# Kernel tuning notes

Measured on AMD Instinct MI355X. Metric: run time of the kernel, lower is better.

The kernel has to match this reference:

```python
import jax, jax.numpy as jnp
import numpy as np

N_NODES = 100000
N_EDGES = 1600000
IN_CH, HID_CH, OUT_CH = 128, 128, 64


def setup_inputs() -> dict:
    key = jax.random.key(0)
    k_x, k_e, k1, k2, k3 = jax.random.split(key, 5)
    x = jax.random.normal(k_x, (N_NODES, IN_CH), dtype=jnp.float32)
    edge_index = jax.random.randint(k_e, (2, N_EDGES), 0, N_NODES, dtype=jnp.int64)
    # Glorot-ish init for the three GCNConv weight matrices (no bias).
    W1 = jax.random.normal(k1, (IN_CH, HID_CH), dtype=jnp.float32) / np.sqrt(IN_CH)
    W2 = jax.random.normal(k2, (HID_CH, HID_CH), dtype=jnp.float32) / np.sqrt(HID_CH)
    W3 = jax.random.normal(k3, (HID_CH, OUT_CH), dtype=jnp.float32) / np.sqrt(HID_CH)
    return {"x": x, "edge_index": edge_index, "W1": W1, "W2": W2, "W3": W3}


def _gcn_layer(x, src, dst, W):
    # GCNConv(normalize=False, bias=False): transform then sum-aggregate over edges.
    h = x @ W                      # [N, d_out]
    msgs = h[src]                  # [E, d_out] gather from source nodes
    return jax.ops.segment_sum(msgs, dst, num_segments=N_NODES)  # scatter-add to targets


def reference(x, edge_index, W1, W2, W3):
    src, dst = edge_index[0], edge_index[1]  # PyG flow: source_to_target
    h = _gcn_layer(x, src, dst, W1)
    h = _gcn_layer(h, src, dst, W2)
    h = _gcn_layer(h, src, dst, W3)
    return h  # [N, OUT_CH]
```

## Files before the change

kernel.cpp:

```cpp
#include <hip/hip_runtime.h>

#define N_NODES 100000
#define N_EDGES 1600000
#define CAP 48
#define NBUCK 256
#define NPB 391
#define SCAP 8192
#define NREP 4
#define SCAP4 (SCAP / NREP)
#define EPB 4096
#define NBIN ((N_EDGES + EPB - 1) / EPB)

typedef unsigned int uint;
typedef unsigned short ushort;

__device__ __forceinline__ void fma4(float4& c, float s, const float4& w) {
    c.x += s * w.x; c.y += s * w.y; c.z += s * w.z; c.w += s * w.w;
}

__device__ __forceinline__ ushort bf16r(float f) {
    union { float f; uint u; } v; v.f = f;
    return (ushort)((v.u + 0x7fffu + ((v.u >> 16) & 1u)) >> 16);
}

struct alignas(16) GemmSmem {
    float Xs[128][36];
    float Ws[32][64];
};

template <typename OutT>
__device__ __forceinline__ void gemm64_block(GemmSmem& sm, int bid,
                                             const float* __restrict__ X,
                                             const float* __restrict__ W,
                                             OutT* __restrict__ H, int n) {
    const int tid  = threadIdx.x;
    const int row0 = bid * 128;
    const int rg   = tid >> 4;
    const int cg   = tid & 15;

    float4 acc0[8];
#pragma unroll
    for (int r = 0; r < 8; r++) acc0[r] = make_float4(0.f, 0.f, 0.f, 0.f);

    const int lr = tid >> 1;
    const int lh = tid & 1;
    int grow = row0 + lr; if (grow > n - 1) grow = n - 1;
    const float* gx_base = X + (size_t)grow * 128 + lh * 16;

    for (int k0 = 0; k0 < 128; k0 += 32) {
        const float* gx = gx_base + k0;
#pragma unroll
        for (int i = 0; i < 4; i++)
            *(float4*)&sm.Xs[lr][lh * 16 + 4 * i] = *(const float4*)(gx + 4 * i);
        const float4* gw = (const float4*)(W + (size_t)k0 * 64);
        float4* sw = (float4*)&sm.Ws[0][0];
#pragma unroll
        for (int i = 0; i < 2; i++) sw[tid + 256 * i] = gw[tid + 256 * i];
        __syncthreads();

#pragma unroll
        for (int kk = 0; kk < 32; kk += 4) {
            float4 w00 = *(const float4*)&sm.Ws[kk + 0][cg * 4];
            float4 w01 = *(const float4*)&sm.Ws[kk + 1][cg * 4];
            float4 w02 = *(const float4*)&sm.Ws[kk + 2][cg * 4];
            float4 w03 = *(const float4*)&sm.Ws[kk + 3][cg * 4];
#pragma unroll
            for (int r = 0; r < 8; r++) {
                float4 a = *(const float4*)&sm.Xs[rg + 16 * r][kk];
                fma4(acc0[r], a.x, w00);
                fma4(acc0[r], a.y, w01);
                fma4(acc0[r], a.z, w02);
                fma4(acc0[r], a.w, w03);
            }
        }
        __syncthreads();
    }

#pragma unroll
    for (int r = 0; r < 8; r++) {
        int row = row0 + rg + 16 * r;
        if (row < n) {
            if constexpr (sizeof(OutT) == 2) {
                ushort4 o0 = make_ushort4(bf16r(acc0[r].x), bf16r(acc0[r].y),
                                          bf16r(acc0[r].z), bf16r(acc0[r].w));
                *(ushort4*)&H[(size_t)row * 64 + cg * 4] = o0;
            } else {
                *(float4*)&H[(size_t)row * 64 + cg * 4] = *(float4*)&acc0[r];
            }
        }
    }
}

union BinWcSmem {
    struct {
        int ecnt[NBUCK];
        int base[NBUCK];
        int lofs[NBUCK];
        uint2 estage[EPB];
    } b;
    GemmSmem g;
};

__global__ void __launch_bounds__(256) bin_wc(const int* __restrict__ src,
                                              const int* __restrict__ dst,
                                              int* __restrict__ gcur,
                                              uint2* __restrict__ seg, int E,
                                              const float* __restrict__ W1,
                                              const float* __restrict__ W2,
                                              const float* __restrict__ W3,
                                              float* __restrict__ W23,
                                              float* __restrict__ Wc) {
    __shared__ BinWcSmem sh;
    if (blockIdx.x == gridDim.x - 1) {
        gemm64_block<float>(sh.g, 0, W2, W3, W23, 128);
        __syncthreads();
        gemm64_block<float>(sh.g, 0, W1, W23, Wc, 128);
        return;
    }
    const int t = threadIdx.x;
    sh.b.ecnt[t] = 0;
    __syncthreads();
    const int e0 = blockIdx.x * EPB;
    const int rep = blockIdx.x & (NREP - 1);
    uint sreg[EPB / 256];
    int  dreg[EPB / 256];
    int  slreg[EPB / 256];
#pragma unroll
    for (int k = 0; k < EPB / 256; k++) {
        int i = e0 + k * 256 + t;
        if (i < E) {
            int d = dst[i];
            sreg[k] = (uint)src[i];
            dreg[k] = d;
            slreg[k] = atomicAdd(&sh.b.ecnt[d / NPB], 1);
        }
    }
    __syncthreads();
    const int c = sh.b.ecnt[t];
    sh.b.base[t] = (c > 0) ? atomicAdd(&gcur[rep * NBUCK + t], c) : 0;
    sh.b.lofs[t] = c;
    __syncthreads();
#pragma unroll
    for (int off = 1; off < NBUCK; off <<= 1) {
        int u = (t >= off) ? sh.b.lofs[t - off] : 0;
        __syncthreads();
        sh.b.lofs[t] += u;
        __syncthreads();
    }
    const int excl = sh.b.lofs[t] - c;
    __syncthreads();
    sh.b.lofs[t] = excl;
    __syncthreads();
#pragma unroll
    for (int k = 0; k < EPB / 256; k++) {
        int i = e0 + k * 256 + t;
        if (i < E) {
            int b = dreg[k] / NPB;
            sh.b.estage[sh.b.lofs[b] + slreg[k]] =
                make_uint2(sreg[k], (uint)dreg[k]);
        }
    }
    __syncthreads();
    const int total = min(E - e0, EPB);
    for (int i = t; i < total; i += 256) {
        uint2 e = sh.b.estage[i];
        int b = (int)e.y / NPB;
        int s = sh.b.base[b] + (i - sh.b.lofs[b]);
        if (s < SCAP4)
            seg[(size_t)b * SCAP + rep * SCAP4 + s] = e;
    }
}

union CsrGemmSmem {
    int lc[NPB];
    GemmSmem g;
};

__global__ void __launch_bounds__(256, 3) csr_gemm(const int* __restrict__ gcur,
                                                   const uint2* __restrict__ seg,
                                                   int* __restrict__ col,
                                                   int* __restrict__ cnt,
                                                   const float* __restrict__ X,
                                                   const float* __restrict__ Wc,
                                                   ushort* __restrict__ Y, int n) {
    __shared__ CsrGemmSmem sh;
    if (blockIdx.x < NBUCK) {
        const int b = blockIdx.x;
        const int t = threadIdx.x;
        for (int i = t; i < NPB; i += 256) sh.lc[i] = 0;
        __syncthreads();
        const int node0 = b * NPB;
#pragma unroll
        for (int q = 0; q < NREP; q++) {
            int m = gcur[q * NBUCK + b]; if (m > SCAP4) m = SCAP4;
            const uint2* sg = seg + (size_t)b * SCAP + q * SCAP4;
            for (int i = t; i < m; i += 256) {
                uint2 e = sg[i];
                int d = (int)e.y;
                int slot = atomicAdd(&sh.lc[d - node0], 1);
                if (slot < CAP) col[(size_t)d * CAP + slot] = (int)e.x;
            }
        }
        __syncthreads();
        for (int i = t; i < NPB; i += 256) {
            int node = node0 + i;
            if (node < n) cnt[node] = (sh.lc[i] > CAP) ? CAP : sh.lc[i];
        }
    } else {
        gemm64_block<ushort>(sh.g, blockIdx.x - NBUCK, X, Wc, Y, n);
    }
}

__device__ __forceinline__ float2 bf2f(uint u) {
    union { uint u; float f; } a, b;
    a.u = u << 16; b.u = u & 0xffff0000u;
    return make_float2(a.f, b.f);
}

template <bool FINAL>
__global__ void __launch_bounds__(256) agg64(const uint4* __restrict__ T_in,
                                             const int* __restrict__ cnt,
                                             const int* __restrict__ col,
                                             void* __restrict__ T_out, int n) {
    int gid  = blockIdx.x * blockDim.x + threadIdx.x;
    int node = gid >> 3;
    int lane = gid & 7;
    if (node >= n) return;
    int m = cnt[node]; if (m > CAP) m = CAP;
    const int* cb = col + (size_t)node * CAP;
    const uint4* tb = T_in + lane;
    float4 accA = make_float4(0.f, 0.f, 0.f, 0.f);
    float4 accB = make_float4(0.f, 0.f, 0.f, 0.f);
    int j = 0;
    for (; j + 8 <= m; j += 8) {
        int4 c0 = *(const int4*)&cb[j];
        int4 c1 = *(const int4*)&cb[j + 4];
        uint4 u0 = tb[(size_t)c0.x * 8];
        uint4 u1 = tb[(size_t)c0.y * 8];
        uint4 u2 = tb[(size_t)c0.z * 8];
        uint4 u3 = tb[(size_t)c0.w * 8];
        uint4 u4 = tb[(size_t)c1.x * 8];
        uint4 u5 = tb[(size_t)c1.y * 8];
        uint4 u6 = tb[(size_t)c1.z * 8];
        uint4 u7 = tb[(size_t)c1.w * 8];
        float2 p0 = bf2f(u0.x), p1 = bf2f(u1.x), p2 = bf2f(u2.x), p3 = bf2f(u3.x);
        float2 p4 = bf2f(u4.x), p5 = bf2f(u5.x), p6 = bf2f(u6.x), p7 = bf2f(u7.x);
        accA.x += ((p0.x + p1.x) + (p2.x + p3.x)) + ((p4.x + p5.x) + (p6.x + p7.x));
        accA.y += ((p0.y + p1.y) + (p2.y + p3.y)) + ((p4.y + p5.y) + (p6.y + p7.y));
        float2 q0 = bf2f(u0.y), q1 = bf2f(u1.y), q2 = bf2f(u2.y), q3 = bf2f(u3.y);
        float2 q4 = bf2f(u4.y), q5 = bf2f(u5.y), q6 = bf2f(u6.y), q7 = bf2f(u7.y);
        accA.z += ((q0.x + q1.x) + (q2.x + q3.x)) + ((q4.x + q5.x) + (q6.x + q7.x));
        accA.w += ((q0.y + q1.y) + (q2.y + q3.y)) + ((q4.y + q5.y) + (q6.y + q7.y));
        float2 r0 = bf2f(u0.z), r1 = bf2f(u1.z), r2 = bf2f(u2.z), r3 = bf2f(u3.z);
        float2 r4 = bf2f(u4.z), r5 = bf2f(u5.z), r6 = bf2f(u6.z), r7 = bf2f(u7.z);
        accB.x += ((r0.x + r1.x) + (r2.x + r3.x)) + ((r4.x + r5.x) + (r6.x + r7.x));
        accB.y += ((r0.y + r1.y) + (r2.y + r3.y)) + ((r4.y + r5.y) + (r6.y + r7.y));
        float2 s0 = bf2f(u0.w), s1 = bf2f(u1.w), s2 = bf2f(u2.w), s3 = bf2f(u3.w);
        float2 s4 = bf2f(u4.w), s5 = bf2f(u5.w), s6 = bf2f(u6.w), s7 = bf2f(u7.w);
        accB.z += ((s0.x + s1.x) + (s2.x + s3.x)) + ((s4.x + s5.x) + (s6.x + s7.x));
        accB.w += ((s0.y + s1.y) + (s2.y + s3.y)) + ((s4.y + s5.y) + (s6.y + s7.y));
    }
    for (; j + 4 <= m; j += 4) {
        int4 c0 = *(const int4*)&cb[j];
        uint4 u0 = tb[(size_t)c0.x * 8];
        uint4 u1 = tb[(size_t)c0.y * 8];
        uint4 u2 = tb[(size_t)c0.z * 8];
        uint4 u3 = tb[(size_t)c0.w * 8];
        float2 p0 = bf2f(u0.x), p1 = bf2f(u1.x), p2 = bf2f(u2.x), p3 = bf2f(u3.x);
        accA.x += (p0.x + p1.x) + (p2.x + p3.x);
        accA.y += (p0.y + p1.y) + (p2.y + p3.y);
        float2 q0 = bf2f(u0.y), q1 = bf2f(u1.y), q2 = bf2f(u2.y), q3 = bf2f(u3.y);
        accA.z += (q0.x + q1.x) + (q2.x + q3.x);
        accA.w += (q0.y + q1.y) + (q2.y + q3.y);
        float2 r0 = bf2f(u0.z), r1 = bf2f(u1.z), r2 = bf2f(u2.z), r3 = bf2f(u3.z);
        accB.x += (r0.x + r1.x) + (r2.x + r3.x);
        accB.y += (r0.y + r1.y) + (r2.y + r3.y);
        float2 s0 = bf2f(u0.w), s1 = bf2f(u1.w), s2 = bf2f(u2.w), s3 = bf2f(u3.w);
        accB.z += (s0.x + s1.x) + (s2.x + s3.x);
        accB.w += (s0.y + s1.y) + (s2.y + s3.y);
    }
    for (; j < m; j++) {
        uint4 u = tb[(size_t)cb[j] * 8];
        float2 p = bf2f(u.x), q = bf2f(u.y), r = bf2f(u.z), s = bf2f(u.w);
        accA.x += p.x; accA.y += p.y; accA.z += q.x; accA.w += q.y;
        accB.x += r.x; accB.y += r.y; accB.z += s.x; accB.w += s.y;
    }
    if (FINAL) {
        ((float4*)T_out)[(size_t)node * 16 + lane * 2]     = accA;
        ((float4*)T_out)[(size_t)node * 16 + lane * 2 + 1] = accB;
    } else {
        uint4 o;
        o.x = (uint)bf16r(accA.x) | ((uint)bf16r(accA.y) << 16);
        o.y = (uint)bf16r(accA.z) | ((uint)bf16r(accA.w) << 16);
        o.z = (uint)bf16r(accB.x) | ((uint)bf16r(accB.y) << 16);
        o.w = (uint)bf16r(accB.z) | ((uint)bf16r(accB.w) << 16);
        ((uint4*)T_out)[(size_t)node * 8 + lane] = o;
    }
}


static inline size_t align_up(size_t x, size_t a) { return (x + a - 1) & ~(a - 1); }

extern "C" void kernel_launch(void* const* d_in, const int* in_sizes, int n_in,
                              void* d_out, int out_size, void* d_ws, size_t ws_size,
                              hipStream_t stream) {
    const float* x  = (const float*)d_in[0];
    const int*   ei = (const int*)d_in[1];
    const float* W1 = (const float*)d_in[2];
    const float* W2 = (const float*)d_in[3];
    const float* W3 = (const float*)d_in[4];
    float* out = (float*)d_out;

    const int N = N_NODES;
    const int E = N_EDGES;
    const int* src = ei;
    const int* dst = ei + E;

    char* p = (char*)d_ws;
    int*    gcur = (int*)p;   p += align_up((size_t)NREP * NBUCK * 4, 256);
    int*    cnt  = (int*)p;   p += align_up((size_t)N * 4, 256);
    uint2*  seg  = (uint2*)p; p += align_up((size_t)NBUCK * SCAP * 8, 256);
    int*    col  = (int*)p;   p += align_up((size_t)N * CAP * 4, 256);
    float*  W23  = (float*)p; p += align_up((size_t)128 * 64 * 4, 256);
    float*  Wc   = (float*)p; p += align_up((size_t)128 * 64 * 4, 256);
    ushort* Y    = (ushort*)p; p += align_up((size_t)N * 64 * 2, 256);
    ushort* Za   = (ushort*)p; p += align_up((size_t)N * 64 * 2, 256);

    hipMemsetAsync(gcur, 0, (size_t)NREP * NBUCK * 4, stream);

    bin_wc<<<NBIN + 1, 256, 0, stream>>>(src, dst, gcur, seg, E,
                                         W1, W2, W3, W23, Wc);

    const int gemm_blocks = (N + 127) / 128;
    csr_gemm<<<NBUCK + gemm_blocks, 256, 0, stream>>>(gcur, seg, col, cnt,
                                                      x, Wc, Y, N);

    const int agg_blocks = (N * 8 + 255) / 256;
    agg64<false><<<agg_blocks, 256, 0, stream>>>((const uint4*)Y,  cnt, col, Za, N);
    agg64<false><<<agg_blocks, 256, 0, stream>>>((const uint4*)Za, cnt, col, Y,  N);
    agg64<true ><<<agg_blocks, 256, 0, stream>>>((const uint4*)Y,  cnt, col, out, N);
}
```

Measured before the change: 251.1 us.

## Replace padded ELL neighbor lists with compact per-bucket CSR rowptr layout

The CSR build now counts in-degrees per bucket first, runs a shared-memory prefix scan (each degree rounded up to a multiple of 4 for int4 loads), and writes neighbor indices compactly into a per-bucket region with a rowptr array, instead of fixed 48-slot padded rows per node. The aggregation kernels read neighbor lists through rowptr. This shrinks the col array and improves cache and DRAM locality of the index reads in the three aggregation passes. In exchange the build does a second pass over the binned edges, an extra scan with several barriers, and one more indirection load per node.

```diff
diff --git a/kernel.cpp b/kernel.cpp
--- a/kernel.cpp
+++ b/kernel.cpp
@@ -172,7 +172,11 @@
 }
 
 union CsrGemmSmem {
-    int lc[NPB];
+    struct {
+        int lc[NPB];
+        int lrp[NPB];
+        int sc[2][512];
+    } c;
     GemmSmem g;
 };
 
@@ -180,6 +184,7 @@
                                                    const uint2* __restrict__ seg,
                                                    int* __restrict__ col,
                                                    int* __restrict__ cnt,
+                                                   int* __restrict__ rowptr,
                                                    const float* __restrict__ X,
                                                    const float* __restrict__ Wc,
                                                    ushort* __restrict__ Y, int n) {
@@ -187,24 +192,59 @@
     if (blockIdx.x < NBUCK) {
         const int b = blockIdx.x;
         const int t = threadIdx.x;
-        for (int i = t; i < NPB; i += 256) sh.lc[i] = 0;
-        __syncthreads();
         const int node0 = b * NPB;
+        for (int i = t; i < NPB; i += 256) sh.c.lc[i] = 0;
+        __syncthreads();
+#pragma unroll
+        for (int q = 0; q < NREP; q++) {
+            int m = gcur[q * NBUCK + b]; if (m > SCAP4) m = SCAP4;
+            const uint2* sg = seg + (size_t)b * SCAP + q * SCAP4;
+            for (int i = t; i < m; i += 256)
+                atomicAdd(&sh.c.lc[(int)sg[i].y - node0], 1);
+        }
+        __syncthreads();
+        sh.c.sc[0][t]       = (t < NPB) ? ((sh.c.lc[t] + 3) & ~3) : 0;
+        sh.c.sc[0][t + 256] = (t + 256 < NPB) ? ((sh.c.lc[t + 256] + 3) & ~3) : 0;
+        __syncthreads();
+        int pb = 0;
+#pragma unroll
+        for (int off = 1; off < 512; off <<= 1) {
+            int a0 = sh.c.sc[pb][t];
+            int a1 = sh.c.sc[pb][t + 256];
+            int b0 = (t >= off) ? sh.c.sc[pb][t - off] : 0;
+            int b1 = (t + 256 >= off) ? sh.c.sc[pb][t + 256 - off] : 0;
+            sh.c.sc[pb ^ 1][t]       = a0 + b0;
+            sh.c.sc[pb ^ 1][t + 256] = a1 + b1;
+            __syncthreads();
+            pb ^= 1;
+        }
+        if (t < NPB)
+            sh.c.lrp[t] = sh.c.sc[pb][t] - ((sh.c.lc[t] + 3) & ~3);
+        if (t + 256 < NPB)
+            sh.c.lrp[t + 256] = sh.c.sc[pb][t + 256] - ((sh.c.lc[t + 256] + 3) & ~3);
+        __syncthreads();
+        for (int i = t; i < NPB; i += 256) sh.c.lc[i] = 0;
+        __syncthreads();
 #pragma unroll
         for (int q = 0; q < NREP; q++) {
             int m = gcur[q * NBUCK + b]; if (m > SCAP4) m = SCAP4;
             const uint2* sg = seg + (size_t)b * SCAP + q * SCAP4;
             for (int i = t; i < m; i += 256) {
                 uint2 e = sg[i];
-                int d = (int)e.y;
-                int slot = atomicAdd(&sh.lc[d - node0], 1);
-                if (slot < CAP) col[(size_t)d * CAP + slot] = (int)e.x;
+                int dn = (int)e.y - node0;
+                int slot = atomicAdd(&sh.c.lc[dn], 1);
+                int pos = sh.c.lrp[dn] + slot;
+                if (pos < SCAP) col[(size_t)b * SCAP + pos] = (int)e.x;
             }
         }
         __syncthreads();
         for (int i = t; i < NPB; i += 256) {
             int node = node0 + i;
-            if (node < n) cnt[node] = (sh.lc[i] > CAP) ? CAP : sh.lc[i];
+            if (node < n) {
+                int c = sh.c.lc[i];
+                cnt[node] = (c > CAP) ? CAP : c;
+                rowptr[node] = b * SCAP + sh.c.lrp[i];
+            }
         }
     } else {
         gemm64_block<ushort>(sh.g, blockIdx.x - NBUCK, X, Wc, Y, n);
@@ -221,13 +261,14 @@
 __global__ void __launch_bounds__(256) agg64(const uint4* __restrict__ T_in,
                                              const int* __restrict__ cnt,
                                              const int* __restrict__ col,
+                                             const int* __restrict__ rowptr,
                                              void* __restrict__ T_out, int n) {
     int gid  = blockIdx.x * blockDim.x + threadIdx.x;
     int node = gid >> 3;
     int lane = gid & 7;
     if (node >= n) return;
     int m = cnt[node]; if (m > CAP) m = CAP;
-    const int* cb = col + (size_t)node * CAP;
+    const int* cb = col + rowptr[node];
     const uint4* tb = T_in + lane;
     float4 accA = make_float4(0.f, 0.f, 0.f, 0.f);
     float4 accB = make_float4(0.f, 0.f, 0.f, 0.f);
@@ -317,14 +358,15 @@
     const int* dst = ei + E;
 
     char* p = (char*)d_ws;
-    int*    gcur = (int*)p;   p += align_up((size_t)NREP * NBUCK * 4, 256);
-    int*    cnt  = (int*)p;   p += align_up((size_t)N * 4, 256);
-    uint2*  seg  = (uint2*)p; p += align_up((size_t)NBUCK * SCAP * 8, 256);
-    int*    col  = (int*)p;   p += align_up((size_t)N * CAP * 4, 256);
-    float*  W23  = (float*)p; p += align_up((size_t)128 * 64 * 4, 256);
-    float*  Wc   = (float*)p; p += align_up((size_t)128 * 64 * 4, 256);
-    ushort* Y    = (ushort*)p; p += align_up((size_t)N * 64 * 2, 256);
-    ushort* Za   = (ushort*)p; p += align_up((size_t)N * 64 * 2, 256);
+    int*    gcur   = (int*)p;   p += align_up((size_t)NREP * NBUCK * 4, 256);
+    int*    cnt    = (int*)p;   p += align_up((size_t)N * 4, 256);
+    int*    rowptr = (int*)p;   p += align_up((size_t)N * 4, 256);
+    uint2*  seg    = (uint2*)p; p += align_up((size_t)NBUCK * SCAP * 8, 256);
+    int*    col    = (int*)p;   p += align_up((size_t)NBUCK * SCAP * 4, 256);
+    float*  W23    = (float*)p; p += align_up((size_t)128 * 64 * 4, 256);
+    float*  Wc     = (float*)p; p += align_up((size_t)128 * 64 * 4, 256);
+    ushort* Y      = (ushort*)p; p += align_up((size_t)N * 64 * 2, 256);
+    ushort* Za     = (ushort*)p; p += align_up((size_t)N * 64 * 2, 256);
 
     hipMemsetAsync(gcur, 0, (size_t)NREP * NBUCK * 4, stream);
 
@@ -333,10 +375,13 @@
 
     const int gemm_blocks = (N + 127) / 128;
     csr_gemm<<<NBUCK + gemm_blocks, 256, 0, stream>>>(gcur, seg, col, cnt,
-                                                      x, Wc, Y, N);
+                                                      rowptr, x, Wc, Y, N);
 
     const int agg_blocks = (N * 8 + 255) / 256;
-    agg64<false><<<agg_blocks, 256, 0, stream>>>((const uint4*)Y,  cnt, col, Za, N);
-    agg64<false><<<agg_blocks, 256, 0, stream>>>((const uint4*)Za, cnt, col, Y,  N);
-    agg64<true ><<<agg_blocks, 256, 0, stream>>>((const uint4*)Y,  cnt, col, out, N);
-}
+    agg64<false><<<agg_blocks, 256, 0, stream>>>((const uint4*)Y,  cnt, col,
+                                                 rowptr, Za, N);
+    agg64<false><<<agg_blocks, 256, 0, stream>>>((const uint4*)Za, cnt, col,
+                                                 rowptr, Y,  N);
+    agg64<true ><<<agg_blocks, 256, 0, stream>>>((const uint4*)Y,  cnt, col,
+                                                 rowptr, out, N);
+}
```

Result: faster. 242.9 us (-3.3%).
